# Performance work log

Measured on AMD Instinct MI355X. Metric: run time of the kernel, lower is better.

Reference implementation:

```python
import jax, jax.numpy as jnp
import numpy as np

N, T, D = 512, 8, 64   # n_stocks, time_length, infeat
ALPHA, BETA = 0.5, 0.1


def setup_inputs() -> dict:
    key = jax.random.key(0)
    ks = jax.random.split(key, 5)
    x = jax.random.normal(ks[0], (N, T, D), jnp.float32)
    # RelationMapping params: fc1 (2D -> D), fc2 (D -> 1); stored as (in, out)
    W1 = jax.random.normal(ks[1], (2 * D, D), jnp.float32) * (1.0 / np.sqrt(2 * D))
    b1 = jnp.zeros((D,), jnp.float32)
    W2 = jax.random.normal(ks[2], (D, 1), jnp.float32) * (1.0 / np.sqrt(D))
    b2 = jnp.zeros((1,), jnp.float32)
    # time-attention parameter a: (T, 1), xavier-ish init
    a = jax.random.normal(ks[3], (T, 1), jnp.float32) * (1.414 * np.sqrt(2.0 / (T + 1)))
    return {"x": x, "W1": W1, "b1": b1, "W2": W2, "b2": b2, "a": a}


def reference(x, W1, b1, W2, b2, a):
    # x: (n, T, d). Original builds cat([x_i, x_j]) of shape (n, n, 2d) per
    # timestep; fc1(cat) decomposes exactly into x_i @ W1a + x_j @ W1b.
    n, t_len, d = x.shape
    W1a, W1b = W1[:d], W1[d:]               # (d, d) each
    L = jnp.einsum('ntd,dh->tnh', x, W1a)    # row (source) projection
    R = jnp.einsum('ntd,dh->tnh', x, W1b)    # col (target) projection
    w2 = W2[:, 0]                            # (d,)

    # time weights: softmax(a) * (1 + alpha * exp(-beta * (T - i - 1)))
    tt = jnp.arange(t_len, dtype=x.dtype)
    decay = 1.0 + ALPHA * jnp.exp(-BETA * (t_len - tt - 1.0))
    w = jax.nn.softmax(a[:, 0], axis=0) * decay  # (T,)

    def step(acc, args):
        Lt, Rt, wt = args
        h = jax.nn.relu(Lt[:, None, :] + Rt[None, :, :] + b1)  # (n, n, d)
        s = jax.nn.relu(h @ w2 + b2[0])                         # (n, n)
        return acc + wt * s, None

    A0 = jnp.zeros((n, n), x.dtype)
    A, _ = jax.lax.scan(step, A0, (L, R, w))
    return A
```

## Files before the change

kernel.cpp:

```cpp
#include <hip/hip_runtime.h>

#define NN 512
#define TT 8
#define DD 64

__global__ __launch_bounds__(256) void k1_proj(const float* __restrict__ x,
                                               const float* __restrict__ W1,
                                               const float* __restrict__ b1,
                                               float* __restrict__ L,
                                               float* __restrict__ R)
{
    int g    = blockIdx.x * 256 + threadIdx.x;
    int c    = g & 127;
    int h    = c & 63;
    int half = c >> 6;
    int pair = g >> 7;
    int n    = pair >> 1;
    int t0   = (pair & 1) * 4;

    float wcol[DD];
    const float* wbase = W1 + (half << 6) * DD + h;
#pragma unroll
    for (int d = 0; d < DD; ++d) wcol[d] = wbase[d << 6];

    float bias = half ? b1[h] : 0.0f;
    float* outbase = half ? R : L;

#pragma unroll
    for (int tt = 0; tt < 4; ++tt) {
        int t = t0 + tt;
        const float4* xr = (const float4*)(x + n * (TT * DD) + t * DD);
        float acc = 0.0f;
#pragma unroll
        for (int d4 = 0; d4 < 16; ++d4) {
            float4 xv = xr[d4];
            acc = fmaf(xv.x, wcol[d4 * 4 + 0], acc);
            acc = fmaf(xv.y, wcol[d4 * 4 + 1], acc);
            acc = fmaf(xv.z, wcol[d4 * 4 + 2], acc);
            acc = fmaf(xv.w, wcol[d4 * 4 + 3], acc);
        }
        outbase[t * (NN * DD) + n * DD + h] = acc + bias;
    }
}

__global__ __launch_bounds__(1024, 4) void k2_main(const float* __restrict__ L,
                                                   const float* __restrict__ R,
                                                   const float* __restrict__ W2,
                                                   const float* __restrict__ b2,
                                                   const float* __restrict__ a,
                                                   float* __restrict__ A)
{
    extern __shared__ float S[];
    float* const w2s = S + 32768;

    const int tid = threadIdx.x;
    const int i0  = blockIdx.y << 5;
    const int j0  = blockIdx.x << 5;

#pragma unroll
    for (int k = 0; k < 8; ++k) {
        int e    = tid + (k << 10);
        int half = e >> 12;
        int q    = e & 4095;
        int t    = q >> 9;
        int w    = q & 511;
        int row  = w >> 4;
        int c4   = w & 15;
        const float* src = half ? (R + t * (NN * DD) + (j0 + row) * DD)
                                : (L + t * (NN * DD) + (i0 + row) * DD);
        float4 v = ((const float4*)src)[c4];
        float* dst = S + (half ? 16384 : 0) + t * 2048 + (row << 6)
                       + ((c4 ^ ((row >> 1) & 7)) << 2);
        *(float4*)dst = v;
    }
    if (tid < 64) w2s[tid] = W2[tid];

    const int g  = tid >> 8;
    const int id = tid & 255;
    float wt0, wt1;
    {
        float av[8];
#pragma unroll
        for (int t = 0; t < 8; ++t) av[t] = a[t];
        float m = av[0];
#pragma unroll
        for (int t = 1; t < 8; ++t) m = fmaxf(m, av[t]);
        float ssum = 0.0f;
#pragma unroll
        for (int t = 0; t < 8; ++t) ssum += expf(av[t] - m);
        float inv = 1.0f / ssum;
        int ta = 2 * g, tb = 2 * g + 1;
        wt0 = expf(av[ta] - m) * inv * (1.0f + 0.5f * expf(-0.1f * (float)(7 - ta)));
        wt1 = expf(av[tb] - m) * inv * (1.0f + 0.5f * expf(-0.1f * (float)(7 - tb)));
    }
    const float b2v = b2[0];

    __syncthreads();

    const int tj = id & 15;
    const int ti = id >> 4;
    const int riL0 = (2 * ti) << 6,     riL1 = (2 * ti + 1) << 6;
    const int riR0 = (2 * tj) << 6,     riR1 = (2 * tj + 1) << 6;
    const int swLb = ti & 7,            swRb = tj & 7;

    float acc00 = 0.f, acc01 = 0.f, acc10 = 0.f, acc11 = 0.f;

#pragma unroll
    for (int tt = 0; tt < 2; ++tt) {
        const int t = 2 * g + tt;
        const float* LB = S + t * 2048;
        const float* RB = S + 16384 + t * 2048;
        float s00 = 0.f, s01 = 0.f, s10 = 0.f, s11 = 0.f;
#pragma unroll
        for (int d4 = 0; d4 < 16; ++d4) {
            const int swL = (d4 ^ swLb) << 2;
            const int swR = (d4 ^ swRb) << 2;
            float4 l0 = *(const float4*)(LB + riL0 + swL);
            float4 l1 = *(const float4*)(LB + riL1 + swL);
            float4 r0 = *(const float4*)(RB + riR0 + swR);
            float4 r1 = *(const float4*)(RB + riR1 + swR);
            float4 wv = *(const float4*)(w2s + (d4 << 2));
            s00 = fmaf(fmaxf(l0.x + r0.x, 0.f), wv.x, s00);
            s01 = fmaf(fmaxf(l0.x + r1.x, 0.f), wv.x, s01);
            s10 = fmaf(fmaxf(l1.x + r0.x, 0.f), wv.x, s10);
            s11 = fmaf(fmaxf(l1.x + r1.x, 0.f), wv.x, s11);
            s00 = fmaf(fmaxf(l0.y + r0.y, 0.f), wv.y, s00);
            s01 = fmaf(fmaxf(l0.y + r1.y, 0.f), wv.y, s01);
            s10 = fmaf(fmaxf(l1.y + r0.y, 0.f), wv.y, s10);
            s11 = fmaf(fmaxf(l1.y + r1.y, 0.f), wv.y, s11);
            s00 = fmaf(fmaxf(l0.z + r0.z, 0.f), wv.z, s00);
            s01 = fmaf(fmaxf(l0.z + r1.z, 0.f), wv.z, s01);
            s10 = fmaf(fmaxf(l1.z + r0.z, 0.f), wv.z, s10);
            s11 = fmaf(fmaxf(l1.z + r1.z, 0.f), wv.z, s11);
            s00 = fmaf(fmaxf(l0.w + r0.w, 0.f), wv.w, s00);
            s01 = fmaf(fmaxf(l0.w + r1.w, 0.f), wv.w, s01);
            s10 = fmaf(fmaxf(l1.w + r0.w, 0.f), wv.w, s10);
            s11 = fmaf(fmaxf(l1.w + r1.w, 0.f), wv.w, s11);
        }
        const float wt = tt ? wt1 : wt0;
        acc00 = fmaf(wt, fmaxf(s00 + b2v, 0.f), acc00);
        acc01 = fmaf(wt, fmaxf(s01 + b2v, 0.f), acc01);
        acc10 = fmaf(wt, fmaxf(s10 + b2v, 0.f), acc10);
        acc11 = fmaf(wt, fmaxf(s11 + b2v, 0.f), acc11);
    }

    __syncthreads();
    if (g > 0) {
        ((float4*)S)[(g - 1) * 256 + id] = make_float4(acc00, acc01, acc10, acc11);
    }
    __syncthreads();
    if (g == 0) {
#pragma unroll
        for (int gg = 0; gg < 3; ++gg) {
            float4 p = ((const float4*)S)[gg * 256 + id];
            acc00 += p.x; acc01 += p.y; acc10 += p.z; acc11 += p.w;
        }
        const int i = i0 + 2 * ti;
        const int j = j0 + 2 * tj;
        *(float2*)(A + i * NN + j)       = make_float2(acc00, acc01);
        *(float2*)(A + (i + 1) * NN + j) = make_float2(acc10, acc11);
    }
}

extern "C" void kernel_launch(void* const* d_in, const int* in_sizes, int n_in,
                              void* d_out, int out_size, void* d_ws, size_t ws_size,
                              hipStream_t stream) {
    const float* x  = (const float*)d_in[0];
    const float* W1 = (const float*)d_in[1];
    const float* b1 = (const float*)d_in[2];
    const float* W2 = (const float*)d_in[3];
    const float* b2 = (const float*)d_in[4];
    const float* a  = (const float*)d_in[5];
    float* A = (float*)d_out;

    float* L = (float*)d_ws;
    float* R = L + NN * TT * DD;

    k1_proj<<<512, 256, 0, stream>>>(x, W1, b1, L, R);

    size_t ldsBytes = (32768 + 64) * sizeof(float);
    k2_main<<<dim3(16, 16), 1024, ldsBytes, stream>>>(L, R, W2, b2, a, A);
}
```

Baseline: 84.54 us.

## Use 512-thread blocks with one wave per timestep and 4x4 register tiles

The main kernel now runs 512 threads per block instead of 1024. Each 64-lane wave owns one timestep and each lane computes a 4x4 output tile instead of 2x2 across two timesteps. This raises the number of FMAs per LDS load (8 float4 loads feed 16 outputs) to cut shared-memory traffic. The cross-timestep reduction goes through LDS with all threads summing 8 partials. The cost is more register pressure from 16 accumulators plus 8 float4 operands, and possible LDS bank conflicts from the new access pattern.

Result: no change. 84.04 us (-0.6%).

```diff
diff --git a/kernel.cpp b/kernel.cpp
--- a/kernel.cpp
+++ b/kernel.cpp
@@ -43,12 +43,12 @@
     }
 }
 
-__global__ __launch_bounds__(1024, 4) void k2_main(const float* __restrict__ L,
-                                                   const float* __restrict__ R,
-                                                   const float* __restrict__ W2,
-                                                   const float* __restrict__ b2,
-                                                   const float* __restrict__ a,
-                                                   float* __restrict__ A)
+__global__ __launch_bounds__(512) void k2_main(const float* __restrict__ L,
+                                               const float* __restrict__ R,
+                                               const float* __restrict__ W2,
+                                               const float* __restrict__ b2,
+                                               const float* __restrict__ a,
+                                               float* __restrict__ A)
 {
     extern __shared__ float S[];
     float* const w2s = S + 32768;
@@ -58,8 +58,8 @@
     const int j0  = blockIdx.x << 5;
 
 #pragma unroll
-    for (int k = 0; k < 8; ++k) {
-        int e    = tid + (k << 10);
+    for (int k = 0; k < 16; ++k) {
+        int e    = tid + (k << 9);
         int half = e >> 12;
         int q    = e & 4095;
         int t    = q >> 9;
@@ -75,9 +75,12 @@
     }
     if (tid < 64) w2s[tid] = W2[tid];
 
-    const int g  = tid >> 8;
-    const int id = tid & 255;
-    float wt0, wt1;
+    const int wv   = tid >> 6;
+    const int lane = tid & 63;
+    const int tjx  = lane & 7;
+    const int tiy  = lane >> 3;
+
+    float wt;
     {
         float av[8];
 #pragma unroll
@@ -88,77 +91,74 @@
         float ssum = 0.0f;
 #pragma unroll
         for (int t = 0; t < 8; ++t) ssum += expf(av[t] - m);
-        float inv = 1.0f / ssum;
-        int ta = 2 * g, tb = 2 * g + 1;
-        wt0 = expf(av[ta] - m) * inv * (1.0f + 0.5f * expf(-0.1f * (float)(7 - ta)));
-        wt1 = expf(av[tb] - m) * inv * (1.0f + 0.5f * expf(-0.1f * (float)(7 - tb)));
+        wt = expf(av[wv] - m) / ssum
+           * (1.0f + 0.5f * expf(-0.1f * (float)(7 - wv)));
     }
     const float b2v = b2[0];
 
     __syncthreads();
 
-    const int tj = id & 15;
-    const int ti = id >> 4;
-    const int riL0 = (2 * ti) << 6,     riL1 = (2 * ti + 1) << 6;
-    const int riR0 = (2 * tj) << 6,     riR1 = (2 * tj + 1) << 6;
-    const int swLb = ti & 7,            swRb = tj & 7;
+    const float* LB = S + wv * 2048;
+    const float* RB = S + 16384 + wv * 2048;
 
-    float acc00 = 0.f, acc01 = 0.f, acc10 = 0.f, acc11 = 0.f;
+    int lbase[4], rbase[4], lsw[4], rsw[4];
+#pragma unroll
+    for (int r = 0; r < 4; ++r) {
+        int li = 4 * tiy + r;
+        int rj = 4 * tjx + r;
+        lbase[r] = li << 6;  lsw[r] = (li >> 1) & 7;
+        rbase[r] = rj << 6;  rsw[r] = (rj >> 1) & 7;
+    }
 
+    float acc[4][4];
 #pragma unroll
-    for (int tt = 0; tt < 2; ++tt) {
-        const int t = 2 * g + tt;
-        const float* LB = S + t * 2048;
-        const float* RB = S + 16384 + t * 2048;
-        float s00 = 0.f, s01 = 0.f, s10 = 0.f, s11 = 0.f;
+    for (int p = 0; p < 4; ++p)
 #pragma unroll
-        for (int d4 = 0; d4 < 16; ++d4) {
-            const int swL = (d4 ^ swLb) << 2;
-            const int swR = (d4 ^ swRb) << 2;
-            float4 l0 = *(const float4*)(LB + riL0 + swL);
-            float4 l1 = *(const float4*)(LB + riL1 + swL);
-            float4 r0 = *(const float4*)(RB + riR0 + swR);
-            float4 r1 = *(const float4*)(RB + riR1 + swR);
-            float4 wv = *(const float4*)(w2s + (d4 << 2));
-            s00 = fmaf(fmaxf(l0.x + r0.x, 0.f), wv.x, s00);
-            s01 = fmaf(fmaxf(l0.x + r1.x, 0.f), wv.x, s01);
-            s10 = fmaf(fmaxf(l1.x + r0.x, 0.f), wv.x, s10);
-            s11 = fmaf(fmaxf(l1.x + r1.x, 0.f), wv.x, s11);
-            s00 = fmaf(fmaxf(l0.y + r0.y, 0.f), wv.y, s00);
-            s01 = fmaf(fmaxf(l0.y + r1.y, 0.f), wv.y, s01);
-            s10 = fmaf(fmaxf(l1.y + r0.y, 0.f), wv.y, s10);
-            s11 = fmaf(fmaxf(l1.y + r1.y, 0.f), wv.y, s11);
-            s00 = fmaf(fmaxf(l0.z + r0.z, 0.f), wv.z, s00);
-            s01 = fmaf(fmaxf(l0.z + r1.z, 0.f), wv.z, s01);
-            s10 = fmaf(fmaxf(l1.z + r0.z, 0.f), wv.z, s10);
-            s11 = fmaf(fmaxf(l1.z + r1.z, 0.f), wv.z, s11);
-            s00 = fmaf(fmaxf(l0.w + r0.w, 0.f), wv.w, s00);
-            s01 = fmaf(fmaxf(l0.w + r1.w, 0.f), wv.w, s01);
-            s10 = fmaf(fmaxf(l1.w + r0.w, 0.f), wv.w, s10);
-            s11 = fmaf(fmaxf(l1.w + r1.w, 0.f), wv.w, s11);
+        for (int q = 0; q < 4; ++q) acc[p][q] = 0.0f;
+
+#pragma unroll 4
+    for (int d4 = 0; d4 < 16; ++d4) {
+        float4 lv[4], rv[4];
+#pragma unroll
+        for (int r = 0; r < 4; ++r)
+            lv[r] = *(const float4*)(LB + lbase[r] + ((d4 ^ lsw[r]) << 2));
+#pragma unroll
+        for (int r = 0; r < 4; ++r)
+            rv[r] = *(const float4*)(RB + rbase[r] + ((d4 ^ rsw[r]) << 2));
+        float4 w4 = *(const float4*)(w2s + (d4 << 2));
+#pragma unroll
+        for (int p = 0; p < 4; ++p) {
+#pragma unroll
+            for (int q = 0; q < 4; ++q) {
+                float s = acc[p][q];
+                s = fmaf(fmaxf(lv[p].x + rv[q].x, 0.f), w4.x, s);
+                s = fmaf(fmaxf(lv[p].y + rv[q].y, 0.f), w4.y, s);
+                s = fmaf(fmaxf(lv[p].z + rv[q].z, 0.f), w4.z, s);
+                s = fmaf(fmaxf(lv[p].w + rv[q].w, 0.f), w4.w, s);
+                acc[p][q] = s;
+            }
         }
-        const float wt = tt ? wt1 : wt0;
-        acc00 = fmaf(wt, fmaxf(s00 + b2v, 0.f), acc00);
-        acc01 = fmaf(wt, fmaxf(s01 + b2v, 0.f), acc01);
-        acc10 = fmaf(wt, fmaxf(s10 + b2v, 0.f), acc10);
-        acc11 = fmaf(wt, fmaxf(s11 + b2v, 0.f), acc11);
     }
 
     __syncthreads();
-    if (g > 0) {
-        ((float4*)S)[(g - 1) * 256 + id] = make_float4(acc00, acc01, acc10, acc11);
+    float* const P = S;
+#pragma unroll
+    for (int p = 0; p < 4; ++p) {
+        float4 v = make_float4(
+            wt * fmaxf(acc[p][0] + b2v, 0.f),
+            wt * fmaxf(acc[p][1] + b2v, 0.f),
+            wt * fmaxf(acc[p][2] + b2v, 0.f),
+            wt * fmaxf(acc[p][3] + b2v, 0.f));
+        *(float4*)(P + (wv << 10) + ((4 * tiy + p) << 5) + (tjx << 2)) = v;
     }
     __syncthreads();
-    if (g == 0) {
+
 #pragma unroll
-        for (int gg = 0; gg < 3; ++gg) {
-            float4 p = ((const float4*)S)[gg * 256 + id];
-            acc00 += p.x; acc01 += p.y; acc10 += p.z; acc11 += p.w;
-        }
-        const int i = i0 + 2 * ti;
-        const int j = j0 + 2 * tj;
-        *(float2*)(A + i * NN + j)       = make_float2(acc00, acc01);
-        *(float2*)(A + (i + 1) * NN + j) = make_float2(acc10, acc11);
+    for (int e = tid; e < 1024; e += 512) {
+        float s = 0.0f;
+#pragma unroll
+        for (int t = 0; t < 8; ++t) s += P[(t << 10) + e];
+        A[(i0 + (e >> 5)) * NN + j0 + (e & 31)] = s;
     }
 }
 
@@ -179,5 +179,5 @@
     k1_proj<<<512, 256, 0, stream>>>(x, W1, b1, L, R);
 
     size_t ldsBytes = (32768 + 64) * sizeof(float);
-    k2_main<<<dim3(16, 16), 1024, ldsBytes, stream>>>(L, R, W2, b2, a, A);
+    k2_main<<<dim3(16, 16), 512, ldsBytes, stream>>>(L, R, W2, b2, a, A);
 }
```
